# Optimization experiments

Hardware: AMD Instinct MI355X
Metric: run time of the kernel (lower is better)

## Reference

```python
import jax, jax.numpy as jnp
import numpy as np
from jax import lax

B, D, K = 256, 128, 8192


def _conv_same(x, w, b):
    # x: [B,C,H,W], w: [O,I,3,3] (torch Conv2d layout), stride 1, padding 1 == SAME
    y = lax.conv_general_dilated(x, w, (1, 1), 'SAME',
                                 dimension_numbers=('NCHW', 'OIHW', 'NCHW'))
    return y + b[None, :, None, None]


def _convT_same(x, w, b):
    # torch ConvTranspose2d(k=3, stride=1, padding=1) with weight [I,O,3,3]
    # == SAME conv with spatially flipped kernel and swapped in/out channels
    wt = jnp.flip(w, axis=(2, 3)).transpose(1, 0, 2, 3)  # -> [O,I,3,3]
    return _conv_same(x, wt, b)


def setup_inputs() -> dict:
    key = jax.random.key(0)
    ks = jax.random.split(key, 12)
    s = 0.05
    return {
        'patch':  jax.random.normal(ks[0], (B, 3, 64, 64), jnp.float32),
        'enc_w1': jax.random.normal(ks[1], (64, 3, 3, 3), jnp.float32) * s,
        'enc_b1': jnp.zeros((64,), jnp.float32),
        'enc_w2': jax.random.normal(ks[2], (D, 64, 3, 3), jnp.float32) * s,
        'enc_b2': jnp.zeros((D,), jnp.float32),
        'emb':    jax.random.normal(ks[3], (K, D), jnp.float32),
        'dec_w1': jax.random.normal(ks[4], (D, 64, 3, 3), jnp.float32) * s,  # ConvT [in,out,k,k]
        'dec_b1': jnp.zeros((64,), jnp.float32),
        'dec_w2': jax.random.normal(ks[5], (64, 64, 3, 3), jnp.float32) * s,
        'dec_b2': jnp.zeros((64,), jnp.float32),
        'dec_w3': jax.random.normal(ks[6], (64, 3, 3, 3), jnp.float32) * s,
        'dec_b3': jnp.zeros((3,), jnp.float32),
    }


def reference(patch, enc_w1, enc_b1, enc_w2, enc_b2, emb,
              dec_w1, dec_b1, dec_w2, dec_b2, dec_w3, dec_b3):
    # ---- encode_patch ----
    h = jax.nn.relu(_conv_same(patch, enc_w1, enc_b1))
    h = _conv_same(h, enc_w2, enc_b2)
    z = jnp.mean(h, axis=(2, 3))  # AdaptiveAvgPool2d((1,1)) + flatten -> [B,D]

    # ---- VQ: cdist + argmin + gather ----
    # argmin over squared L2 == argmin over cdist(p=2); avoid sqrt.
    d2 = (jnp.sum(z * z, axis=1, keepdims=True)
          + jnp.sum(emb * emb, axis=1)[None, :]
          - 2.0 * z @ emb.T)  # [B,K]
    encoding_indices = jnp.argmin(d2, axis=1)  # [B]
    z_q = emb[encoding_indices]  # [B,D]

    commitment_loss = jnp.mean((lax.stop_gradient(z_q) - z) ** 2)
    codebook_loss = jnp.mean((z_q - lax.stop_gradient(z)) ** 2)

    # ---- decode_vector ----
    # bilinear interpolate of a 1x1 map to 64x64 is a pure broadcast
    v = jnp.broadcast_to(z_q[:, :, None, None], (z_q.shape[0], z_q.shape[1], 64, 64))
    d = jax.nn.relu(_convT_same(v, dec_w1, dec_b1))
    d = jax.nn.relu(_convT_same(d, dec_w2, dec_b2))
    recon = jnp.tanh(_convT_same(d, dec_w3, dec_b3))  # [B,3,64,64]

    return recon, codebook_loss, commitment_loss, encoding_indices[:, None]
```

## Files before the change

### kernel.cpp

```cpp
#include <hip/hip_runtime.h>
#include <math.h>


__global__ __launch_bounds__(256) void k_conv1_stats(
    const float* __restrict__ patch, const float* __restrict__ w1,
    const float* __restrict__ b1, float* __restrict__ pstat)
{
    __shared__ float lds[3 * 18 * 68];
    const int blk = blockIdx.x;
    const int b = blk >> 2, rg = blk & 3;
    const int y0 = rg * 16;
    const int tid = threadIdx.x;

    const float* pb = patch + (size_t)b * 3 * 64 * 64;
    for (int i = tid; i < 3 * 18 * 68; i += 256) {
        int c = i / 1224, rem = i % 1224;
        int r = rem / 68, pc = rem % 68;
        int y = y0 + r - 1, x = pc - 1;
        float v = 0.f;
        if (y >= 0 && y < 64 && x >= 0 && x < 64)
            v = pb[(c << 12) + (y << 6) + x];
        lds[i] = v;
    }
    __syncthreads();

    const int ch = tid & 63;
    const int q  = tid >> 6;

    float w[3][3][3];
#pragma unroll
    for (int ic = 0; ic < 3; ++ic)
#pragma unroll
        for (int ky = 0; ky < 3; ++ky)
#pragma unroll
            for (int kx = 0; kx < 3; ++kx)
                w[ic][ky][kx] = w1[((ch * 3 + ic) * 3 + ky) * 3 + kx];
    const float bias = b1[ch];

    float T = 0, r0 = 0, r63 = 0, c0 = 0, c63 = 0;
    float h00 = 0, h063 = 0, h630 = 0, h6363 = 0;

    for (int yl = q * 4; yl < q * 4 + 4; ++yl) {
        const int y = y0 + yl;
        for (int xc = 0; xc < 16; ++xc) {
            float a0 = bias, a1 = bias, a2 = bias, a3 = bias;
#pragma unroll
            for (int ic = 0; ic < 3; ++ic) {
#pragma unroll
                for (int ky = 0; ky < 3; ++ky) {
                    const float* p = &lds[(ic * 18 + yl + ky) * 68 + xc * 4];
                    float4 va = *(const float4*)p;
                    float2 vb = *(const float2*)(p + 4);
                    float win[6] = {va.x, va.y, va.z, va.w, vb.x, vb.y};
#pragma unroll
                    for (int kx = 0; kx < 3; ++kx) {
                        float wv = w[ic][ky][kx];
                        a0 = fmaf(wv, win[kx + 0], a0);
                        a1 = fmaf(wv, win[kx + 1], a1);
                        a2 = fmaf(wv, win[kx + 2], a2);
                        a3 = fmaf(wv, win[kx + 3], a3);
                    }
                }
            }
            a0 = fmaxf(a0, 0.f); a1 = fmaxf(a1, 0.f);
            a2 = fmaxf(a2, 0.f); a3 = fmaxf(a3, 0.f);
            float rs = a0 + a1 + a2 + a3;
            T += rs;
            if (y == 0)  { r0  += rs; if (xc == 0) h00  = a0; if (xc == 15) h063  = a3; }
            if (y == 63) { r63 += rs; if (xc == 0) h630 = a0; if (xc == 15) h6363 = a3; }
            if (xc == 0)  c0  += a0;
            if (xc == 15) c63 += a3;
        }
    }
    __syncthreads();

    float* red = lds;
    float st[9] = {T, r0, r63, c0, c63, h00, h063, h630, h6363};
#pragma unroll
    for (int s = 0; s < 9; ++s) red[(s * 4 + q) * 64 + ch] = st[s];
    __syncthreads();

    if (tid < 64) {
        float* pp = pstat + (size_t)blk * 576;
#pragma unroll
        for (int s = 0; s < 9; ++s)
            pp[s * 64 + tid] = red[(s * 4 + 0) * 64 + tid] + red[(s * 4 + 1) * 64 + tid]
                             + red[(s * 4 + 2) * 64 + tid] + red[(s * 4 + 3) * 64 + tid];
    }
}

__global__ __launch_bounds__(256) void k_pre(
    const float* __restrict__ dw1, const float* __restrict__ emb,
    float* __restrict__ Wcfg, float* __restrict__ en2)
{
    int gid = blockIdx.x * 256 + threadIdx.x;
    if (gid < 73728) {
        int cfg = gid >> 13;
        int o = (gid >> 7) & 63;
        int i = gid & 127;
        int cy = cfg / 3, cx = cfg % 3;
        int ylo = (cy == 2) ? 1 : 0, yhi = (cy == 0) ? 1 : 2;
        int xlo = (cx == 2) ? 1 : 0, xhi = (cx == 0) ? 1 : 2;
        const float* wp = dw1 + ((size_t)i * 64 + o) * 9;
        float s = 0.f;
        for (int ky = ylo; ky <= yhi; ++ky)
            for (int kx = xlo; kx <= xhi; ++kx)
                s += wp[ky * 3 + kx];
        Wcfg[gid] = s;
    } else if (gid < 73728 + 8192) {
        int k = gid - 73728;
        const float4* e = (const float4*)(emb + (size_t)k * 128);
        float s = 0.f;
        for (int t = 0; t < 32; ++t) {
            float4 v = e[t];
            s = fmaf(v.x, v.x, fmaf(v.y, v.y, fmaf(v.z, v.z, fmaf(v.w, v.w, s))));
        }
        en2[k] = s;
    }
}

__global__ __launch_bounds__(256) void k_zred(
    const float* __restrict__ pstat, const float* __restrict__ w2,
    const float* __restrict__ b2, float* __restrict__ z)
{
    __shared__ float fst[576];
    __shared__ __align__(16) float Ssh[576];
    __shared__ float zp[256];
    const int b = blockIdx.x, tid = threadIdx.x;

    const float* pp = pstat + (size_t)b * 4 * 576;
    for (int i = tid; i < 576; i += 256)
        fst[i] = pp[i] + pp[i + 576] + pp[i + 1152] + pp[i + 1728];
    __syncthreads();

    if (tid < 64) {
        int ch = tid;
        float Tt   = fst[0 * 64 + ch], R0  = fst[1 * 64 + ch], R63 = fst[2 * 64 + ch];
        float C0   = fst[3 * 64 + ch], C63 = fst[4 * 64 + ch];
        float H00  = fst[5 * 64 + ch], H063 = fst[6 * 64 + ch];
        float H630 = fst[7 * 64 + ch], H6363 = fst[8 * 64 + ch];
#pragma unroll
        for (int ky = 0; ky < 3; ++ky) {
            float rex = (ky == 0) ? R63 : (ky == 2 ? R0 : 0.f);
#pragma unroll
            for (int kx = 0; kx < 3; ++kx) {
                float cex = (kx == 0) ? C63 : (kx == 2 ? C0 : 0.f);
                float corner = 0.f;
                if (ky == 0 && kx == 0) corner = H6363;
                if (ky == 0 && kx == 2) corner = H630;
                if (ky == 2 && kx == 0) corner = H063;
                if (ky == 2 && kx == 2) corner = H00;
                Ssh[ch * 9 + ky * 3 + kx] = (Tt - rex - cex + corner) * (1.f / 4096.f);
            }
        }
    }
    __syncthreads();

    const int oc = tid & 127, h = tid >> 7;
    const float4* Wv = (const float4*)(w2 + (size_t)oc * 576 + h * 288);
    const float4* Sv = (const float4*)(Ssh + h * 288);
    float acc = 0.f;
    for (int t = 0; t < 72; ++t) {
        float4 w4 = Wv[t], s4 = Sv[t];
        acc = fmaf(w4.x, s4.x, acc);
        acc = fmaf(w4.y, s4.y, acc);
        acc = fmaf(w4.z, s4.z, acc);
        acc = fmaf(w4.w, s4.w, acc);
    }
    zp[tid] = acc;
    __syncthreads();
    if (tid < 128) z[(size_t)b * 128 + tid] = b2[tid] + zp[tid] + zp[tid + 128];
}

__global__ __launch_bounds__(256) void k_vq_partial(
    const float* __restrict__ z, const float* __restrict__ emb,
    const float* __restrict__ en2,
    float* __restrict__ pd2, int* __restrict__ pidx)
{
    __shared__ __align__(16) float zsh[512];
    __shared__ float wd[4][4];
    __shared__ int   wi[4][4];
    const int tid = threadIdx.x;
    const int bg = blockIdx.x >> 4, kc = blockIdx.x & 15;
    const int b0 = bg * 4;
    for (int i = tid; i < 512; i += 256) zsh[i] = z[(size_t)b0 * 128 + i];
    __syncthreads();

    const int k0 = kc * 512 + tid;
    const float4* zv = (const float4*)zsh;
    const float4* e0 = (const float4*)(emb + (size_t)k0 * 128);
    const float4* e1 = (const float4*)(emb + (size_t)(k0 + 256) * 128);

    float acc0[4] = {0, 0, 0, 0}, acc1[4] = {0, 0, 0, 0};
    for (int t = 0; t < 32; ++t) {
        float4 ea = e0[t], eb = e1[t];
#pragma unroll
        for (int bb = 0; bb < 4; ++bb) {
            float4 zz = zv[bb * 32 + t];
            acc0[bb] = fmaf(zz.x, ea.x, fmaf(zz.y, ea.y, fmaf(zz.z, ea.z, fmaf(zz.w, ea.w, acc0[bb]))));
            acc1[bb] = fmaf(zz.x, eb.x, fmaf(zz.y, eb.y, fmaf(zz.z, eb.z, fmaf(zz.w, eb.w, acc1[bb]))));
        }
    }
    const float E0 = en2[k0], E1 = en2[k0 + 256];

#pragma unroll
    for (int bb = 0; bb < 4; ++bb) {
        float da = E0 - 2.f * acc0[bb];
        float db = E1 - 2.f * acc1[bb];
        float d; int ix;
        if (da <= db) { d = da; ix = k0; } else { d = db; ix = k0 + 256; }
#pragma unroll
        for (int off = 32; off > 0; off >>= 1) {
            float od = __shfl_xor(d, off);
            int   oi = __shfl_xor(ix, off);
            if (od < d || (od == d && oi < ix)) { d = od; ix = oi; }
        }
        if ((tid & 63) == 0) { wd[bb][tid >> 6] = d; wi[bb][tid >> 6] = ix; }
    }
    __syncthreads();
    if (tid < 4) {
        int bb = tid;
        float d = wd[bb][0]; int ix = wi[bb][0];
#pragma unroll
        for (int wv = 1; wv < 4; ++wv) {
            float od = wd[bb][wv]; int oi = wi[bb][wv];
            if (od < d || (od == d && oi < ix)) { d = od; ix = oi; }
        }
        pd2[(b0 + bb) * 16 + kc] = d;
        pidx[(b0 + bb) * 16 + kc] = ix;
    }
}

__global__ __launch_bounds__(256) void k_vq_final(
    const float* __restrict__ z, const float* __restrict__ emb,
    const float* __restrict__ pd2, const int* __restrict__ pidx,
    float* __restrict__ zq, float* __restrict__ out)
{
    __shared__ float red[256];
    const int b = threadIdx.x;
    float best = 1e30f; int bi = 0x7fffffff;
    for (int kc = 0; kc < 16; ++kc) {
        float d = pd2[b * 16 + kc]; int ix = pidx[b * 16 + kc];
        if (d < best || (d == best && ix < bi)) { best = d; bi = ix; }
    }
    out[3145730 + b] = (float)bi;
    float ss = 0.f;
    const float4* e  = (const float4*)(emb + (size_t)bi * 128);
    const float4* zb = (const float4*)(z + (size_t)b * 128);
    float4* zqb = (float4*)(zq + (size_t)b * 128);
    for (int t = 0; t < 32; ++t) {
        float4 ev = e[t], zz = zb[t];
        zqb[t] = ev;
        float dx = ev.x - zz.x, dy = ev.y - zz.y, dz = ev.z - zz.z, dw = ev.w - zz.w;
        ss = fmaf(dx, dx, fmaf(dy, dy, fmaf(dz, dz, fmaf(dw, dw, ss))));
    }
    red[b] = ss;
    __syncthreads();
    for (int s = 128; s > 0; s >>= 1) {
        if (b < s) red[b] += red[b + s];
        __syncthreads();
    }
    if (b == 0) {
        float l = red[0] / 32768.f;
        out[3145728] = l;
        out[3145729] = l;
    }
}

__global__ __launch_bounds__(256) void k_decode(
    const float* __restrict__ zq, const float* __restrict__ Wcfg,
    const float* __restrict__ db1, const float* __restrict__ dw2,
    const float* __restrict__ db2, const float* __restrict__ dw3,
    const float* __restrict__ db3, float* __restrict__ out)
{
    __shared__ __align__(16) float zsh[128];
    __shared__ float d1e[64][10];
    __shared__ float d2e[64][26];
    __shared__ float o3[3 * 49];

    const int b = blockIdx.x, tid = threadIdx.x;
    if (tid < 128) zsh[tid] = zq[(size_t)b * 128 + tid];
    if (tid < 64) { d1e[tid][9] = 0.f; d2e[tid][25] = 0.f; }
    __syncthreads();

    for (int id = tid; id < 576; id += 256) {
        int o = id / 9, cfg = id % 9;
        const float4* wv = (const float4*)(Wcfg + ((size_t)cfg * 64 + o) * 128);
        const float4* zv = (const float4*)zsh;
        float acc = db1[o];
        for (int t = 0; t < 32; ++t) {
            float4 w4 = wv[t], z4 = zv[t];
            acc = fmaf(w4.x, z4.x, acc);
            acc = fmaf(w4.y, z4.y, acc);
            acc = fmaf(w4.z, z4.z, acc);
            acc = fmaf(w4.w, z4.w, acc);
        }
        d1e[o][cfg] = fmaxf(acc, 0.f);
    }
    __syncthreads();

    {
        const int TY5[5][3] = {{-1,0,1},{0,1,1},{1,1,1},{1,1,2},{1,2,-1}};
        const int o = tid >> 2, isub = tid & 3;
        float acc[25];
#pragma unroll
        for (int c = 0; c < 25; ++c) acc[c] = 0.f;
        for (int ii = 0; ii < 16; ++ii) {
            int i = isub + ii * 4;
            float d1v[10];
#pragma unroll
            for (int t = 0; t < 9; ++t) d1v[t] = d1e[i][t];
            d1v[9] = 0.f;
            float w9[9];
            const float* wp = dw2 + ((size_t)i * 64 + o) * 9;
#pragma unroll
            for (int t = 0; t < 9; ++t) w9[t] = wp[t];
#pragma unroll
            for (int cy = 0; cy < 5; ++cy) {
#pragma unroll
                for (int ky = 0; ky < 3; ++ky) {
                    int ty = TY5[cy][ky];
                    if (ty < 0) continue;
#pragma unroll
                    for (int cx = 0; cx < 5; ++cx) {
#pragma unroll
                        for (int kx = 0; kx < 3; ++kx) {
                            int tx = TY5[cx][kx];
                            if (tx < 0) continue;
                            acc[cy * 5 + cx] = fmaf(w9[(2 - ky) * 3 + (2 - kx)],
                                                    d1v[ty * 3 + tx], acc[cy * 5 + cx]);
                        }
                    }
                }
            }
        }
#pragma unroll
        for (int c = 0; c < 25; ++c) {
            float v = acc[c];
            v += __shfl_xor(v, 1);
            v += __shfl_xor(v, 2);
            if (isub == 0) d2e[o][c] = fmaxf(v + db2[o], 0.f);
        }
    }
    __syncthreads();

    if (tid < 147) {
        const int TY7[7][3] = {{-1,0,1},{0,1,2},{1,2,2},{2,2,2},{2,2,3},{2,3,4},{3,4,-1}};
        int c3 = tid / 49, cc = tid % 49, cy = cc / 7, cx = cc % 7;
        float acc = db3[c3];
        for (int i = 0; i < 64; ++i) {
            const float* wp = dw3 + ((size_t)i * 3 + c3) * 9;
#pragma unroll
            for (int ky = 0; ky < 3; ++ky) {
                int ty = TY7[cy][ky];
#pragma unroll
                for (int kx = 0; kx < 3; ++kx) {
                    int tx = TY7[cx][kx];
                    int t = (ty < 0 || tx < 0) ? 25 : ty * 5 + tx;
                    acc = fmaf(wp[(2 - ky) * 3 + (2 - kx)], d2e[i][t], acc);
                }
            }
        }
        o3[c3 * 49 + cc] = tanhf(acc);
    }
    __syncthreads();

    float4* ob = (float4*)(out + (size_t)b * 3 * 4096);
    for (int id = tid; id < 3072; id += 256) {
        int base = id * 4;
        int c = base >> 12, rem = base & 4095, y = rem >> 6, x0 = rem & 63;
        int ry = (y <= 3) ? y : (y >= 60 ? y - 57 : 3);
        const float* row = &o3[c * 49 + ry * 7];
        float4 v;
        int x;
        x = x0 + 0; v.x = row[(x <= 3) ? x : (x >= 60 ? x - 57 : 3)];
        x = x0 + 1; v.y = row[(x <= 3) ? x : (x >= 60 ? x - 57 : 3)];
        x = x0 + 2; v.z = row[(x <= 3) ? x : (x >= 60 ? x - 57 : 3)];
        x = x0 + 3; v.w = row[(x <= 3) ? x : (x >= 60 ? x - 57 : 3)];
        ob[id] = v;
    }
}

extern "C" void kernel_launch(void* const* d_in, const int* in_sizes, int n_in,
                              void* d_out, int out_size, void* d_ws, size_t ws_size,
                              hipStream_t stream)
{
    const float* patch  = (const float*)d_in[0];
    const float* enc_w1 = (const float*)d_in[1];
    const float* enc_b1 = (const float*)d_in[2];
    const float* enc_w2 = (const float*)d_in[3];
    const float* enc_b2 = (const float*)d_in[4];
    const float* emb    = (const float*)d_in[5];
    const float* dec_w1 = (const float*)d_in[6];
    const float* dec_b1 = (const float*)d_in[7];
    const float* dec_w2 = (const float*)d_in[8];
    const float* dec_b2 = (const float*)d_in[9];
    const float* dec_w3 = (const float*)d_in[10];
    const float* dec_b3 = (const float*)d_in[11];

    float* out = (float*)d_out;
    float* ws  = (float*)d_ws;

    float* pstat = ws;
    float* z     = ws + 589824;
    float* zq    = ws + 622592;
    float* pd2   = ws + 655360;
    int*   pidx  = (int*)(ws + 659456);
    float* Wcfg  = ws + 663552;
    float* en2   = ws + 737280;

    k_conv1_stats<<<dim3(1024), dim3(256), 0, stream>>>(patch, enc_w1, enc_b1, pstat);
    k_pre<<<dim3(320), dim3(256), 0, stream>>>(dec_w1, emb, Wcfg, en2);
    k_zred<<<dim3(256), dim3(256), 0, stream>>>(pstat, enc_w2, enc_b2, z);
    k_vq_partial<<<dim3(1024), dim3(256), 0, stream>>>(z, emb, en2, pd2, pidx);
    k_vq_final<<<dim3(1), dim3(256), 0, stream>>>(z, emb, pd2, pidx, zq, out);
    k_decode<<<dim3(256), dim3(256), 0, stream>>>(zq, Wcfg, dec_b1, dec_w2, dec_b2,
                                                  dec_w3, dec_b3, out);
}
```

Before: 159.4 us.

## Merge precompute into conv1, fold VQ final into decode, enlarge VQ batch tiles

The precompute kernel is merged into the conv1 stats kernel as extra blocks. The conv1 stage now uses 8-row tiles (2048 blocks) with a register sliding window that reuses the overlapping input columns. The single-block VQ-final kernel is removed. Each decode block redoes the 16-way argmin reduction, gathers its codeword directly, and computes the loss from a precomputed ||z||^2 plus the min distance. The VQ partial kernel processes 16 batch rows per block instead of 4, so each embedding row is loaded fewer times, at the cost of more registers and fewer blocks.

```diff
diff --git a/kernel.cpp b/kernel.cpp
--- a/kernel.cpp
+++ b/kernel.cpp
@@ -2,21 +2,51 @@
 #include <math.h>
 
 
-__global__ __launch_bounds__(256) void k_conv1_stats(
+__global__ __launch_bounds__(256) void k_conv1_pre(
     const float* __restrict__ patch, const float* __restrict__ w1,
-    const float* __restrict__ b1, float* __restrict__ pstat)
+    const float* __restrict__ b1, const float* __restrict__ dw1,
+    const float* __restrict__ emb, float* __restrict__ pstat,
+    float* __restrict__ Wcfg, float* __restrict__ en2)
 {
-    __shared__ float lds[3 * 18 * 68];
+    __shared__ __align__(16) float lds[2304];
     const int blk = blockIdx.x;
-    const int b = blk >> 2, rg = blk & 3;
-    const int y0 = rg * 16;
     const int tid = threadIdx.x;
 
-    const float* pb = patch + (size_t)b * 3 * 64 * 64;
-    for (int i = tid; i < 3 * 18 * 68; i += 256) {
-        int c = i / 1224, rem = i % 1224;
-        int r = rem / 68, pc = rem % 68;
-        int y = y0 + r - 1, x = pc - 1;
+    if (blk >= 2048) {
+        const int gid = (blk - 2048) * 256 + tid;
+        if (gid < 73728) {
+            const int cfg = gid >> 13;
+            const int o = (gid >> 7) & 63;
+            const int i = gid & 127;
+            const int cy = cfg / 3, cx = cfg % 3;
+            const int ylo = (cy == 2) ? 1 : 0, yhi = (cy == 0) ? 1 : 2;
+            const int xlo = (cx == 2) ? 1 : 0, xhi = (cx == 0) ? 1 : 2;
+            const float* wp = dw1 + ((size_t)i * 64 + o) * 9;
+            float s = 0.f;
+            for (int ky = ylo; ky <= yhi; ++ky)
+                for (int kx = xlo; kx <= xhi; ++kx)
+                    s += wp[ky * 3 + kx];
+            Wcfg[gid] = s;
+        } else if (gid < 81920) {
+            const int k = gid - 73728;
+            const float4* e = (const float4*)(emb + (size_t)k * 128);
+            float s = 0.f;
+            for (int t = 0; t < 32; ++t) {
+                float4 v = e[t];
+                s = fmaf(v.x, v.x, fmaf(v.y, v.y, fmaf(v.z, v.z, fmaf(v.w, v.w, s))));
+            }
+            en2[k] = s;
+        }
+        return;
+    }
+
+    const int b = blk >> 3, rg = blk & 7;
+    const int y0 = rg * 8;
+    const float* pb = patch + (size_t)b * 12288;
+    for (int i = tid; i < 2160; i += 256) {
+        const int c = i / 720, rem = i - c * 720;
+        const int r = rem / 72, p = rem - r * 72;
+        const int y = y0 + r - 1, x = p - 3;
         float v = 0.f;
         if (y >= 0 && y < 64 && x >= 0 && x < 64)
             v = pb[(c << 12) + (y << 6) + x];
@@ -24,9 +54,7 @@
     }
     __syncthreads();
 
-    const int ch = tid & 63;
-    const int q  = tid >> 6;
-
+    const int ch = tid & 63, q = tid >> 6;
     float w[3][3][3];
 #pragma unroll
     for (int ic = 0; ic < 3; ++ic)
@@ -37,114 +65,92 @@
                 w[ic][ky][kx] = w1[((ch * 3 + ic) * 3 + ky) * 3 + kx];
     const float bias = b1[ch];
 
-    float T = 0, r0 = 0, r63 = 0, c0 = 0, c63 = 0;
+    float T = 0, r0s = 0, r63s = 0, c0s = 0, c63s = 0;
     float h00 = 0, h063 = 0, h630 = 0, h6363 = 0;
 
-    for (int yl = q * 4; yl < q * 4 + 4; ++yl) {
-        const int y = y0 + yl;
+#pragma unroll
+    for (int sub = 0; sub < 2; ++sub) {
+        const int yl = q * 2 + sub;
+        const bool isr0  = (rg == 0) && (yl == 0);
+        const bool isr63 = (rg == 7) && (yl == 7);
+        float cr[3][3][2];
+#pragma unroll
+        for (int ic = 0; ic < 3; ++ic)
+#pragma unroll
+            for (int ky = 0; ky < 3; ++ky) {
+                const float2 t2 = *(const float2*)&lds[(ic * 10 + yl + ky) * 72 + 2];
+                cr[ic][ky][0] = t2.x; cr[ic][ky][1] = t2.y;
+            }
+#pragma unroll 4
         for (int xc = 0; xc < 16; ++xc) {
             float a0 = bias, a1 = bias, a2 = bias, a3 = bias;
 #pragma unroll
-            for (int ic = 0; ic < 3; ++ic) {
+            for (int ic = 0; ic < 3; ++ic)
 #pragma unroll
                 for (int ky = 0; ky < 3; ++ky) {
-                    const float* p = &lds[(ic * 18 + yl + ky) * 68 + xc * 4];
-                    float4 va = *(const float4*)p;
-                    float2 vb = *(const float2*)(p + 4);
-                    float win[6] = {va.x, va.y, va.z, va.w, vb.x, vb.y};
-#pragma unroll
-                    for (int kx = 0; kx < 3; ++kx) {
-                        float wv = w[ic][ky][kx];
-                        a0 = fmaf(wv, win[kx + 0], a0);
-                        a1 = fmaf(wv, win[kx + 1], a1);
-                        a2 = fmaf(wv, win[kx + 2], a2);
-                        a3 = fmaf(wv, win[kx + 3], a3);
-                    }
+                    const float4 nw = *(const float4*)&lds[(ic * 10 + yl + ky) * 72 + xc * 4 + 4];
+                    const float w0 = w[ic][ky][0], w1v = w[ic][ky][1], w2v = w[ic][ky][2];
+                    a0 = fmaf(w0, cr[ic][ky][0], fmaf(w1v, cr[ic][ky][1], fmaf(w2v, nw.x, a0)));
+                    a1 = fmaf(w0, cr[ic][ky][1], fmaf(w1v, nw.x, fmaf(w2v, nw.y, a1)));
+                    a2 = fmaf(w0, nw.x, fmaf(w1v, nw.y, fmaf(w2v, nw.z, a2)));
+                    a3 = fmaf(w0, nw.y, fmaf(w1v, nw.z, fmaf(w2v, nw.w, a3)));
+                    cr[ic][ky][0] = nw.z; cr[ic][ky][1] = nw.w;
                 }
-            }
             a0 = fmaxf(a0, 0.f); a1 = fmaxf(a1, 0.f);
             a2 = fmaxf(a2, 0.f); a3 = fmaxf(a3, 0.f);
-            float rs = a0 + a1 + a2 + a3;
+            const float rs = (a0 + a1) + (a2 + a3);
             T += rs;
-            if (y == 0)  { r0  += rs; if (xc == 0) h00  = a0; if (xc == 15) h063  = a3; }
-            if (y == 63) { r63 += rs; if (xc == 0) h630 = a0; if (xc == 15) h6363 = a3; }
-            if (xc == 0)  c0  += a0;
-            if (xc == 15) c63 += a3;
-        }
-    }
-    __syncthreads();
-
-    float* red = lds;
-    float st[9] = {T, r0, r63, c0, c63, h00, h063, h630, h6363};
-#pragma unroll
-    for (int s = 0; s < 9; ++s) red[(s * 4 + q) * 64 + ch] = st[s];
-    __syncthreads();
-
+            if (isr0)  { r0s += rs;  if (xc == 0) h00 = a0;  if (xc == 15) h063 = a3; }
+            if (isr63) { r63s += rs; if (xc == 0) h630 = a0; if (xc == 15) h6363 = a3; }
+            if (xc == 0)  c0s += a0;
+            if (xc == 15) c63s += a3;
+        }
+    }
+    __syncthreads();
+    float st[9] = {T, r0s, r63s, c0s, c63s, h00, h063, h630, h6363};
+#pragma unroll
+    for (int s = 0; s < 9; ++s) lds[(s * 4 + q) * 64 + ch] = st[s];
+    __syncthreads();
     if (tid < 64) {
         float* pp = pstat + (size_t)blk * 576;
 #pragma unroll
         for (int s = 0; s < 9; ++s)
-            pp[s * 64 + tid] = red[(s * 4 + 0) * 64 + tid] + red[(s * 4 + 1) * 64 + tid]
-                             + red[(s * 4 + 2) * 64 + tid] + red[(s * 4 + 3) * 64 + tid];
-    }
-}
-
-__global__ __launch_bounds__(256) void k_pre(
-    const float* __restrict__ dw1, const float* __restrict__ emb,
-    float* __restrict__ Wcfg, float* __restrict__ en2)
-{
-    int gid = blockIdx.x * 256 + threadIdx.x;
-    if (gid < 73728) {
-        int cfg = gid >> 13;
-        int o = (gid >> 7) & 63;
-        int i = gid & 127;
-        int cy = cfg / 3, cx = cfg % 3;
-        int ylo = (cy == 2) ? 1 : 0, yhi = (cy == 0) ? 1 : 2;
-        int xlo = (cx == 2) ? 1 : 0, xhi = (cx == 0) ? 1 : 2;
-        const float* wp = dw1 + ((size_t)i * 64 + o) * 9;
-        float s = 0.f;
-        for (int ky = ylo; ky <= yhi; ++ky)
-            for (int kx = xlo; kx <= xhi; ++kx)
-                s += wp[ky * 3 + kx];
-        Wcfg[gid] = s;
-    } else if (gid < 73728 + 8192) {
-        int k = gid - 73728;
-        const float4* e = (const float4*)(emb + (size_t)k * 128);
-        float s = 0.f;
-        for (int t = 0; t < 32; ++t) {
-            float4 v = e[t];
-            s = fmaf(v.x, v.x, fmaf(v.y, v.y, fmaf(v.z, v.z, fmaf(v.w, v.w, s))));
-        }
-        en2[k] = s;
+            pp[s * 64 + tid] = lds[(s * 4 + 0) * 64 + tid] + lds[(s * 4 + 1) * 64 + tid]
+                             + lds[(s * 4 + 2) * 64 + tid] + lds[(s * 4 + 3) * 64 + tid];
     }
 }
 
 __global__ __launch_bounds__(256) void k_zred(
     const float* __restrict__ pstat, const float* __restrict__ w2,
-    const float* __restrict__ b2, float* __restrict__ z)
+    const float* __restrict__ b2, float* __restrict__ z, float* __restrict__ zn2)
 {
     __shared__ float fst[576];
     __shared__ __align__(16) float Ssh[576];
     __shared__ float zp[256];
+    __shared__ float red2[128];
     const int b = blockIdx.x, tid = threadIdx.x;
 
-    const float* pp = pstat + (size_t)b * 4 * 576;
-    for (int i = tid; i < 576; i += 256)
-        fst[i] = pp[i] + pp[i + 576] + pp[i + 1152] + pp[i + 1728];
+    const float* pp = pstat + (size_t)b * 8 * 576;
+    for (int i = tid; i < 576; i += 256) {
+        float s = 0.f;
+#pragma unroll
+        for (int g = 0; g < 8; ++g) s += pp[g * 576 + i];
+        fst[i] = s;
+    }
     __syncthreads();
 
     if (tid < 64) {
-        int ch = tid;
-        float Tt   = fst[0 * 64 + ch], R0  = fst[1 * 64 + ch], R63 = fst[2 * 64 + ch];
-        float C0   = fst[3 * 64 + ch], C63 = fst[4 * 64 + ch];
-        float H00  = fst[5 * 64 + ch], H063 = fst[6 * 64 + ch];
-        float H630 = fst[7 * 64 + ch], H6363 = fst[8 * 64 + ch];
+        const int ch = tid;
+        const float Tt   = fst[0 * 64 + ch], R0  = fst[1 * 64 + ch], R63 = fst[2 * 64 + ch];
+        const float C0   = fst[3 * 64 + ch], C63 = fst[4 * 64 + ch];
+        const float H00  = fst[5 * 64 + ch], H063 = fst[6 * 64 + ch];
+        const float H630 = fst[7 * 64 + ch], H6363 = fst[8 * 64 + ch];
 #pragma unroll
         for (int ky = 0; ky < 3; ++ky) {
-            float rex = (ky == 0) ? R63 : (ky == 2 ? R0 : 0.f);
+            const float rex = (ky == 0) ? R63 : (ky == 2 ? R0 : 0.f);
 #pragma unroll
             for (int kx = 0; kx < 3; ++kx) {
-                float cex = (kx == 0) ? C63 : (kx == 2 ? C0 : 0.f);
+                const float cex = (kx == 0) ? C63 : (kx == 2 ? C0 : 0.f);
                 float corner = 0.f;
                 if (ky == 0 && kx == 0) corner = H6363;
                 if (ky == 0 && kx == 2) corner = H630;
@@ -161,7 +167,7 @@
     const float4* Sv = (const float4*)(Ssh + h * 288);
     float acc = 0.f;
     for (int t = 0; t < 72; ++t) {
-        float4 w4 = Wv[t], s4 = Sv[t];
+        const float4 w4 = Wv[t], s4 = Sv[t];
         acc = fmaf(w4.x, s4.x, acc);
         acc = fmaf(w4.y, s4.y, acc);
         acc = fmaf(w4.z, s4.z, acc);
@@ -169,127 +175,129 @@
     }
     zp[tid] = acc;
     __syncthreads();
-    if (tid < 128) z[(size_t)b * 128 + tid] = b2[tid] + zp[tid] + zp[tid + 128];
+    if (tid < 128) {
+        const float zv = b2[tid] + zp[tid] + zp[tid + 128];
+        z[(size_t)b * 128 + tid] = zv;
+        red2[tid] = zv * zv;
+    }
+    __syncthreads();
+    if (tid < 64) {
+        float v = red2[tid] + red2[tid + 64];
+        v += __shfl_xor(v, 32); v += __shfl_xor(v, 16); v += __shfl_xor(v, 8);
+        v += __shfl_xor(v, 4);  v += __shfl_xor(v, 2);  v += __shfl_xor(v, 1);
+        if (tid == 0) zn2[b] = v;
+    }
 }
 
-__global__ __launch_bounds__(256) void k_vq_partial(
+__global__ __launch_bounds__(256) void k_vq(
     const float* __restrict__ z, const float* __restrict__ emb,
-    const float* __restrict__ en2,
-    float* __restrict__ pd2, int* __restrict__ pidx)
+    const float* __restrict__ en2, float* __restrict__ pd2, int* __restrict__ pidx)
 {
-    __shared__ __align__(16) float zsh[512];
-    __shared__ float wd[4][4];
-    __shared__ int   wi[4][4];
+    __shared__ __align__(16) float zsh[2048];
+    __shared__ float wd[16][4];
+    __shared__ int   wi[16][4];
     const int tid = threadIdx.x;
     const int bg = blockIdx.x >> 4, kc = blockIdx.x & 15;
-    const int b0 = bg * 4;
-    for (int i = tid; i < 512; i += 256) zsh[i] = z[(size_t)b0 * 128 + i];
-    __syncthreads();
-
-    const int k0 = kc * 512 + tid;
+    const int b0 = bg * 16;
+    for (int i = tid; i < 2048; i += 256) zsh[i] = z[(size_t)b0 * 128 + i];
+    __syncthreads();
+
+    const int k0 = kc * 512 + tid, k1 = k0 + 256;
+    const float4* e0 = (const float4*)(emb + (size_t)k0 * 128);
+    const float4* e1 = (const float4*)(emb + (size_t)k1 * 128);
     const float4* zv = (const float4*)zsh;
-    const float4* e0 = (const float4*)(emb + (size_t)k0 * 128);
-    const float4* e1 = (const float4*)(emb + (size_t)(k0 + 256) * 128);
-
-    float acc0[4] = {0, 0, 0, 0}, acc1[4] = {0, 0, 0, 0};
+
+    float acc0[16], acc1[16];
+#pragma unroll
+    for (int bb = 0; bb < 16; ++bb) { acc0[bb] = 0.f; acc1[bb] = 0.f; }
+
     for (int t = 0; t < 32; ++t) {
-        float4 ea = e0[t], eb = e1[t];
-#pragma unroll
-        for (int bb = 0; bb < 4; ++bb) {
-            float4 zz = zv[bb * 32 + t];
+        const float4 ea = e0[t], eb = e1[t];
+#pragma unroll
+        for (int bb = 0; bb < 16; ++bb) {
+            const float4 zz = zv[bb * 32 + t];
             acc0[bb] = fmaf(zz.x, ea.x, fmaf(zz.y, ea.y, fmaf(zz.z, ea.z, fmaf(zz.w, ea.w, acc0[bb]))));
             acc1[bb] = fmaf(zz.x, eb.x, fmaf(zz.y, eb.y, fmaf(zz.z, eb.z, fmaf(zz.w, eb.w, acc1[bb]))));
         }
     }
-    const float E0 = en2[k0], E1 = en2[k0 + 256];
-
-#pragma unroll
-    for (int bb = 0; bb < 4; ++bb) {
-        float da = E0 - 2.f * acc0[bb];
-        float db = E1 - 2.f * acc1[bb];
+    const float E0 = en2[k0], E1 = en2[k1];
+    const int wv_ = tid >> 6, ln = tid & 63;
+#pragma unroll
+    for (int bb = 0; bb < 16; ++bb) {
+        const float da = fmaf(-2.f, acc0[bb], E0);
+        const float db = fmaf(-2.f, acc1[bb], E1);
         float d; int ix;
-        if (da <= db) { d = da; ix = k0; } else { d = db; ix = k0 + 256; }
+        if (da <= db) { d = da; ix = k0; } else { d = db; ix = k1; }
 #pragma unroll
         for (int off = 32; off > 0; off >>= 1) {
-            float od = __shfl_xor(d, off);
-            int   oi = __shfl_xor(ix, off);
+            const float od = __shfl_xor(d, off);
+            const int   oi = __shfl_xor(ix, off);
             if (od < d || (od == d && oi < ix)) { d = od; ix = oi; }
         }
-        if ((tid & 63) == 0) { wd[bb][tid >> 6] = d; wi[bb][tid >> 6] = ix; }
-    }
-    __syncthreads();
-    if (tid < 4) {
-        int bb = tid;
-        float d = wd[bb][0]; int ix = wi[bb][0];
-#pragma unroll
-        for (int wv = 1; wv < 4; ++wv) {
-            float od = wd[bb][wv]; int oi = wi[bb][wv];
+        if (ln == 0) { wd[bb][wv_] = d; wi[bb][wv_] = ix; }
+    }
+    __syncthreads();
+    if (tid < 16) {
+        float d = wd[tid][0]; int ix = wi[tid][0];
+#pragma unroll
+        for (int wv2 = 1; wv2 < 4; ++wv2) {
+            const float od = wd[tid][wv2]; const int oi = wi[tid][wv2];
             if (od < d || (od == d && oi < ix)) { d = od; ix = oi; }
         }
-        pd2[(b0 + bb) * 16 + kc] = d;
-        pidx[(b0 + bb) * 16 + kc] = ix;
+        pd2[(b0 + tid) * 16 + kc] = d;
+        pidx[(b0 + tid) * 16 + kc] = ix;
     }
 }
 
-__global__ __launch_bounds__(256) void k_vq_final(
-    const float* __restrict__ z, const float* __restrict__ emb,
+__global__ __launch_bounds__(256) void k_decode(
+    const float* __restrict__ emb, const float* __restrict__ zn2,
     const float* __restrict__ pd2, const int* __restrict__ pidx,
-    float* __restrict__ zq, float* __restrict__ out)
-{
-    __shared__ float red[256];
-    const int b = threadIdx.x;
-    float best = 1e30f; int bi = 0x7fffffff;
-    for (int kc = 0; kc < 16; ++kc) {
-        float d = pd2[b * 16 + kc]; int ix = pidx[b * 16 + kc];
-        if (d < best || (d == best && ix < bi)) { best = d; bi = ix; }
-    }
-    out[3145730 + b] = (float)bi;
-    float ss = 0.f;
-    const float4* e  = (const float4*)(emb + (size_t)bi * 128);
-    const float4* zb = (const float4*)(z + (size_t)b * 128);
-    float4* zqb = (float4*)(zq + (size_t)b * 128);
-    for (int t = 0; t < 32; ++t) {
-        float4 ev = e[t], zz = zb[t];
-        zqb[t] = ev;
-        float dx = ev.x - zz.x, dy = ev.y - zz.y, dz = ev.z - zz.z, dw = ev.w - zz.w;
-        ss = fmaf(dx, dx, fmaf(dy, dy, fmaf(dz, dz, fmaf(dw, dw, ss))));
-    }
-    red[b] = ss;
-    __syncthreads();
-    for (int s = 128; s > 0; s >>= 1) {
-        if (b < s) red[b] += red[b + s];
-        __syncthreads();
-    }
-    if (b == 0) {
-        float l = red[0] / 32768.f;
-        out[3145728] = l;
-        out[3145729] = l;
-    }
-}
-
-__global__ __launch_bounds__(256) void k_decode(
-    const float* __restrict__ zq, const float* __restrict__ Wcfg,
-    const float* __restrict__ db1, const float* __restrict__ dw2,
-    const float* __restrict__ db2, const float* __restrict__ dw3,
-    const float* __restrict__ db3, float* __restrict__ out)
+    const float* __restrict__ Wcfg, const float* __restrict__ db1,
+    const float* __restrict__ dw2, const float* __restrict__ db2,
+    const float* __restrict__ dw3, const float* __restrict__ db3,
+    float* __restrict__ out)
 {
     __shared__ __align__(16) float zsh[128];
     __shared__ float d1e[64][10];
     __shared__ float d2e[64][26];
     __shared__ float o3[3 * 49];
+    __shared__ int   bisld[256];
+    __shared__ float redl[256];
 
     const int b = blockIdx.x, tid = threadIdx.x;
-    if (tid < 128) zsh[tid] = zq[(size_t)b * 128 + tid];
-    if (tid < 64) { d1e[tid][9] = 0.f; d2e[tid][25] = 0.f; }
-    __syncthreads();
+
+    float dmin = pd2[tid * 16]; int bi = pidx[tid * 16];
+    for (int j = 1; j < 16; ++j) {
+        const float d = pd2[tid * 16 + j]; const int ix = pidx[tid * 16 + j];
+        if (d < dmin || (d == dmin && ix < bi)) { dmin = d; bi = ix; }
+    }
+    bisld[tid] = bi;
+    redl[tid] = dmin + zn2[tid];
+    __syncthreads();
+
+    const int mybi = bisld[b];
+    if (tid < 128) { zsh[tid] = emb[(size_t)mybi * 128 + tid]; redl[tid] += redl[tid + 128]; }
+    if (tid >= 128 && tid < 192) { d1e[tid - 128][9] = 0.f; d2e[tid - 128][25] = 0.f; }
+    __syncthreads();
+    if (tid < 64) {
+        float v = redl[tid] + redl[tid + 64];
+        v += __shfl_xor(v, 32); v += __shfl_xor(v, 16); v += __shfl_xor(v, 8);
+        v += __shfl_xor(v, 4);  v += __shfl_xor(v, 2);  v += __shfl_xor(v, 1);
+        if (tid == 0 && b == 0) {
+            const float L = v * (1.f / 32768.f);
+            out[3145728] = L;
+            out[3145729] = L;
+        }
+    }
+    if (b == 0) out[3145730 + tid] = (float)bisld[tid];
 
     for (int id = tid; id < 576; id += 256) {
-        int o = id / 9, cfg = id % 9;
+        const int o = id / 9, cfg = id % 9;
         const float4* wv = (const float4*)(Wcfg + ((size_t)cfg * 64 + o) * 128);
         const float4* zv = (const float4*)zsh;
         float acc = db1[o];
         for (int t = 0; t < 32; ++t) {
-            float4 w4 = wv[t], z4 = zv[t];
+            const float4 w4 = wv[t], z4 = zv[t];
             acc = fmaf(w4.x, z4.x, acc);
             acc = fmaf(w4.y, z4.y, acc);
             acc = fmaf(w4.z, z4.z, acc);
@@ -306,7 +314,7 @@
 #pragma unroll
         for (int c = 0; c < 25; ++c) acc[c] = 0.f;
         for (int ii = 0; ii < 16; ++ii) {
-            int i = isub + ii * 4;
+            const int i = isub + ii * 4;
             float d1v[10];
 #pragma unroll
             for (int t = 0; t < 9; ++t) d1v[t] = d1e[i][t];
@@ -319,13 +327,13 @@
             for (int cy = 0; cy < 5; ++cy) {
 #pragma unroll
                 for (int ky = 0; ky < 3; ++ky) {
-                    int ty = TY5[cy][ky];
+                    const int ty = TY5[cy][ky];
                     if (ty < 0) continue;
 #pragma unroll
                     for (int cx = 0; cx < 5; ++cx) {
 #pragma unroll
                         for (int kx = 0; kx < 3; ++kx) {
-                            int tx = TY5[cx][kx];
+                            const int tx = TY5[cx][kx];
                             if (tx < 0) continue;
                             acc[cy * 5 + cx] = fmaf(w9[(2 - ky) * 3 + (2 - kx)],
                                                     d1v[ty * 3 + tx], acc[cy * 5 + cx]);
@@ -346,17 +354,17 @@
 
     if (tid < 147) {
         const int TY7[7][3] = {{-1,0,1},{0,1,2},{1,2,2},{2,2,2},{2,2,3},{2,3,4},{3,4,-1}};
-        int c3 = tid / 49, cc = tid % 49, cy = cc / 7, cx = cc % 7;
+        const int c3 = tid / 49, cc = tid % 49, cy = cc / 7, cx = cc % 7;
         float acc = db3[c3];
         for (int i = 0; i < 64; ++i) {
             const float* wp = dw3 + ((size_t)i * 3 + c3) * 9;
 #pragma unroll
             for (int ky = 0; ky < 3; ++ky) {
-                int ty = TY7[cy][ky];
+                const int ty = TY7[cy][ky];
 #pragma unroll
                 for (int kx = 0; kx < 3; ++kx) {
-                    int tx = TY7[cx][kx];
-                    int t = (ty < 0 || tx < 0) ? 25 : ty * 5 + tx;
+                    const int tx = TY7[cx][kx];
+                    const int t = (ty < 0 || tx < 0) ? 25 : ty * 5 + tx;
                     acc = fmaf(wp[(2 - ky) * 3 + (2 - kx)], d2e[i][t], acc);
                 }
             }
@@ -365,11 +373,11 @@
     }
     __syncthreads();
 
-    float4* ob = (float4*)(out + (size_t)b * 3 * 4096);
+    float4* ob = (float4*)(out + (size_t)b * 12288);
     for (int id = tid; id < 3072; id += 256) {
-        int base = id * 4;
-        int c = base >> 12, rem = base & 4095, y = rem >> 6, x0 = rem & 63;
-        int ry = (y <= 3) ? y : (y >= 60 ? y - 57 : 3);
+        const int base = id * 4;
+        const int c = base >> 12, rem = base & 4095, y = rem >> 6, x0 = rem & 63;
+        const int ry = (y <= 3) ? y : (y >= 60 ? y - 57 : 3);
         const float* row = &o3[c * 49 + ry * 7];
         float4 v;
         int x;
@@ -402,18 +410,17 @@
     float* ws  = (float*)d_ws;
 
     float* pstat = ws;
-    float* z     = ws + 589824;
-    float* zq    = ws + 622592;
-    float* pd2   = ws + 655360;
-    int*   pidx  = (int*)(ws + 659456);
-    float* Wcfg  = ws + 663552;
-    float* en2   = ws + 737280;
-
-    k_conv1_stats<<<dim3(1024), dim3(256), 0, stream>>>(patch, enc_w1, enc_b1, pstat);
-    k_pre<<<dim3(320), dim3(256), 0, stream>>>(dec_w1, emb, Wcfg, en2);
-    k_zred<<<dim3(256), dim3(256), 0, stream>>>(pstat, enc_w2, enc_b2, z);
-    k_vq_partial<<<dim3(1024), dim3(256), 0, stream>>>(z, emb, en2, pd2, pidx);
-    k_vq_final<<<dim3(1), dim3(256), 0, stream>>>(z, emb, pd2, pidx, zq, out);
-    k_decode<<<dim3(256), dim3(256), 0, stream>>>(zq, Wcfg, dec_b1, dec_w2, dec_b2,
-                                                  dec_w3, dec_b3, out);
+    float* z     = ws + 1179648;
+    float* zn2   = ws + 1212416;
+    float* pd2   = ws + 1212672;
+    int*   pidx  = (int*)(ws + 1216768);
+    float* Wcfg  = ws + 1220864;
+    float* en2   = ws + 1294592;
+
+    k_conv1_pre<<<dim3(2368), dim3(256), 0, stream>>>(patch, enc_w1, enc_b1, dec_w1,
+                                                      emb, pstat, Wcfg, en2);
+    k_zred<<<dim3(256), dim3(256), 0, stream>>>(pstat, enc_w2, enc_b2, z, zn2);
+    k_vq<<<dim3(256), dim3(256), 0, stream>>>(z, emb, en2, pd2, pidx);
+    k_decode<<<dim3(256), dim3(256), 0, stream>>>(emb, zn2, pd2, pidx, Wcfg, dec_b1,
+                                                  dec_w2, dec_b2, dec_w3, dec_b3, out);
 }
```

After: 131.3 us. 1.21x faster.
